# Kernel optimization log

Hardware: AMD Instinct MI355X
Metric: run time of the kernel (lower is better)

## Reference

```python
import jax, jax.numpy as jnp
import numpy as np

TOP_K = 2  # n_heads / k in SigmaMoE


def setup_inputs() -> dict:
    key = jax.random.key(0)
    k1, k2, k3, k4 = jax.random.split(key, 4)
    B, S, d = 4, 2048, 512
    E, H = 32, 128  # n_experts, expert_size
    # init scales mirror reset_parameters (std ~ 1/sqrt(fan_in)) so sigmoid router is unsaturated
    x = jax.random.normal(k1, (B, S, d), dtype=jnp.float32)
    expert_sel = jax.random.normal(k2, (E, d), dtype=jnp.float32) / np.sqrt(d).astype(np.float32)
    keys = jax.random.normal(k3, (E, d, H), dtype=jnp.float32) / np.sqrt(d).astype(np.float32)
    values = jax.random.normal(k4, (E, H, d), dtype=jnp.float32) / np.sqrt(E * H).astype(np.float32)
    return {"x": x, "expert_sel": expert_sel, "keys": keys, "values": values}


def reference(x, expert_sel, keys, values):
    # x: [B, S, d]; expert_sel: [E, d]; keys: [E, d, H]; values: [E, H, v]
    B, S, d = x.shape
    E = keys.shape[0]
    xt = x.reshape(-1, d)                       # [T, d] tokens
    T = xt.shape[0]

    # Router: sigmoid gate + top-k expert selection (eval mode: no dropout, no sel_hist)
    sel = jax.nn.sigmoid(xt @ expert_sel.T)     # [T, E]
    sel_val, sel_idx = jax.lax.top_k(sel, TOP_K)  # [T, K] each; combine is order-invariant

    # Sparse routing weights as dense [T, E] mask (zero for unselected experts,
    # so unselected expert compute is exactly cancelled -> same math as cvmm dispatch/combine)
    w = jnp.zeros((T, E), dtype=xt.dtype).at[jnp.arange(T)[:, None], sel_idx].add(sel_val)

    # Expert FFN: scores = relu(x @ keys[e]); out = sum_e w[t,e] * scores @ values[e]
    h = jax.nn.relu(jnp.einsum('td,edh->teh', xt, keys))   # [T, E, H]
    out = jnp.einsum('teh,te,ehv->tv', h, w, values)       # [T, v]
    return out.reshape(B, S, -1)
```

## Files before the change

### kernel.cpp

```cpp
#include <hip/hip_runtime.h>

#define TT 8192
#define DD 512
#define EE 32
#define HH 128

typedef float f32x4 __attribute__((ext_vector_type(4)));
typedef __bf16 bf16x8 __attribute__((ext_vector_type(8)));
typedef unsigned short u16x8 __attribute__((ext_vector_type(8)));

__device__ __forceinline__ unsigned short f2bf(float f) {
  unsigned int u = __builtin_bit_cast(unsigned int, f);
  u = (u + 0x7FFFu + ((u >> 16) & 1u)) >> 16;
  return (unsigned short)u;
}
__device__ __forceinline__ float bf2f(unsigned short h) {
  return __builtin_bit_cast(float, (unsigned int)h << 16);
}

#define GLD16(g, l)                                                            \
  __builtin_amdgcn_global_load_lds(                                            \
      (const __attribute__((address_space(1))) unsigned int*)(g),              \
      (__attribute__((address_space(3))) unsigned int*)(l), 16, 0, 0)

__global__ __launch_bounds__(256) void convert_kernel(
    const float* __restrict__ keys, const float* __restrict__ values,
    const float* __restrict__ esel,
    unsigned short* __restrict__ keysT, unsigned short* __restrict__ valuesT,
    unsigned short* __restrict__ eselF, int* __restrict__ cur) {
  __shared__ float tile[64][68];
  int bid = blockIdx.x;
  const int t = threadIdx.x;
  if (bid >= 1024) {
    if (bid == 1024 && t < EE) cur[t] = 0;
    int f = (bid - 1024) * 256 + t;
    int lane = f & 63;
    int rest = f >> 6;
    int half = rest & 1;
    int kt = rest >> 1;
    int term = kt % 3;
    int k = kt / 3;
    int n = half * 16 + (lane & 15);
    int col = k * 32 + (lane >> 4) * 8;
    const float* s = esel + (size_t)n * DD + col;
    unsigned short o[8];
#pragma unroll
    for (int q = 0; q < 8; q++) {
      float v = s[q];
      unsigned short hh = f2bf(v);
      float r1 = v - bf2f(hh);
      unsigned short lo = f2bf(r1);
      float r2 = r1 - bf2f(lo);
      o[q] = (term == 0) ? hh : (term == 1) ? lo : f2bf(r2);
    }
    *(u16x8*)(eselF + (size_t)f * 8) = *(const u16x8*)o;
    return;
  }
  const float* src;
  unsigned short* dst;
  int R, C, r0, c0, e;
  if (bid < 512) {
    e = bid >> 4; int sub = bid & 15;
    R = DD; C = HH; r0 = (sub >> 1) * 64; c0 = (sub & 1) * 64;
    src = keys; dst = keysT;
  } else {
    bid -= 512;
    e = bid >> 4; int sub = bid & 15;
    R = HH; C = DD; r0 = (sub & 1) * 64; c0 = (sub >> 1) * 64;
    src = values; dst = valuesT;
  }
  const int rl = t >> 2, cq = (t & 3) * 16;
  const float* s0 = src + ((size_t)e * R + r0 + rl) * C + c0 + cq;
#pragma unroll
  for (int i = 0; i < 4; i++) *(float4*)&tile[rl][cq + 4 * i] = *(const float4*)(s0 + 4 * i);
  __syncthreads();
  unsigned short* d0 = dst + ((size_t)e * C + c0 + rl) * R + r0 + cq;
#pragma unroll
  for (int i = 0; i < 4; i++) {
    ushort4 v;
    v.x = f2bf(tile[cq + 4 * i + 0][rl]);
    v.y = f2bf(tile[cq + 4 * i + 1][rl]);
    v.z = f2bf(tile[cq + 4 * i + 2][rl]);
    v.w = f2bf(tile[cq + 4 * i + 3][rl]);
    *(ushort4*)(d0 + 4 * i) = v;
  }
}

__global__ __launch_bounds__(256) void router_kernel(
    const float* __restrict__ x, const unsigned short* __restrict__ eselF,
    unsigned short* __restrict__ xb, int* __restrict__ etok,
    float* __restrict__ ew, int* __restrict__ cur) {
  __shared__ float ls[2][32][33];
  __shared__ int bcnt[EE], bbase[EE], bcur[EE];
  const int tid = threadIdx.x;
  const int tok0 = blockIdx.x * 32;
  const int wv = tid >> 6, lane = tid & 63;
  const int mh = wv & 1;
  const int kh2 = wv >> 1;
  const int ll = lane & 15, lh = lane >> 4;
  const int row = tok0 + mh * 16 + ll;

  const float* xr = x + (size_t)row * DD + lh * 8;
  unsigned short* xbr = xb + (size_t)row * DD + lh * 8;

  f32x4 acc0, acc1;
  acc0[0] = 0.f; acc0[1] = 0.f; acc0[2] = 0.f; acc0[3] = 0.f;
  acc1 = acc0;

  for (int kl = 0; kl < 8; kl++) {
    int k = kh2 * 8 + kl;
    float4 v0 = *(const float4*)(xr + k * 32);
    float4 v1 = *(const float4*)(xr + k * 32 + 4);
    float vv[8] = {v0.x, v0.y, v0.z, v0.w, v1.x, v1.y, v1.z, v1.w};
    bf16x8 ah, al, al2;
    unsigned short hs[8];
#pragma unroll
    for (int j = 0; j < 8; j++) {
      unsigned short hh = f2bf(vv[j]);
      float r1 = vv[j] - bf2f(hh);
      unsigned short lo = f2bf(r1);
      float r2 = r1 - bf2f(lo);
      hs[j] = hh;
      ah[j] = __builtin_bit_cast(__bf16, hh);
      al[j] = __builtin_bit_cast(__bf16, lo);
      al2[j] = __builtin_bit_cast(__bf16, f2bf(r2));
    }
    *(ushort4*)(xbr + k * 32) = *(ushort4*)&hs[0];
    *(ushort4*)(xbr + k * 32 + 4) = *(ushort4*)&hs[4];

    const unsigned short* fk = eselF + (size_t)k * 6 * 512 + lane * 8;
    bf16x8 bh0 = *(const bf16x8*)(fk);
    bf16x8 bh1 = *(const bf16x8*)(fk + 512);
    bf16x8 bl0 = *(const bf16x8*)(fk + 1024);
    bf16x8 bl1 = *(const bf16x8*)(fk + 1536);
    bf16x8 bm0 = *(const bf16x8*)(fk + 2048);
    bf16x8 bm1 = *(const bf16x8*)(fk + 2560);

    acc0 = __builtin_amdgcn_mfma_f32_16x16x32_bf16(ah, bh0, acc0, 0, 0, 0);
    acc0 = __builtin_amdgcn_mfma_f32_16x16x32_bf16(ah, bl0, acc0, 0, 0, 0);
    acc0 = __builtin_amdgcn_mfma_f32_16x16x32_bf16(al, bh0, acc0, 0, 0, 0);
    acc0 = __builtin_amdgcn_mfma_f32_16x16x32_bf16(ah, bm0, acc0, 0, 0, 0);
    acc0 = __builtin_amdgcn_mfma_f32_16x16x32_bf16(al, bl0, acc0, 0, 0, 0);
    acc0 = __builtin_amdgcn_mfma_f32_16x16x32_bf16(al2, bh0, acc0, 0, 0, 0);

    acc1 = __builtin_amdgcn_mfma_f32_16x16x32_bf16(ah, bh1, acc1, 0, 0, 0);
    acc1 = __builtin_amdgcn_mfma_f32_16x16x32_bf16(ah, bl1, acc1, 0, 0, 0);
    acc1 = __builtin_amdgcn_mfma_f32_16x16x32_bf16(al, bh1, acc1, 0, 0, 0);
    acc1 = __builtin_amdgcn_mfma_f32_16x16x32_bf16(ah, bm1, acc1, 0, 0, 0);
    acc1 = __builtin_amdgcn_mfma_f32_16x16x32_bf16(al, bl1, acc1, 0, 0, 0);
    acc1 = __builtin_amdgcn_mfma_f32_16x16x32_bf16(al2, bh1, acc1, 0, 0, 0);
  }

#pragma unroll
  for (int r = 0; r < 4; r++) {
    ls[kh2][mh * 16 + lh * 4 + r][ll] = acc0[r];
    ls[kh2][mh * 16 + lh * 4 + r][16 + ll] = acc1[r];
  }
  if (tid < EE) bcnt[tid] = 0;
  __syncthreads();

  int i0 = 0, i1 = 0;
  float w0 = 0.f, w1 = 0.f;
  if (tid < 32) {
    float m0 = -3.4e38f;
#pragma unroll
    for (int e2 = 0; e2 < EE; e2++) {
      float v = ls[0][tid][e2] + ls[1][tid][e2];
      if (v > m0) { m0 = v; i0 = e2; }
    }
    float m1 = -3.4e38f;
    i1 = (i0 == 0) ? 1 : 0;
#pragma unroll
    for (int e2 = 0; e2 < EE; e2++) {
      float v = ls[0][tid][e2] + ls[1][tid][e2];
      if (e2 != i0 && v > m1) { m1 = v; i1 = e2; }
    }
    w0 = 1.f / (1.f + expf(-m0));
    w1 = 1.f / (1.f + expf(-m1));
    atomicAdd(&bcnt[i0], 1);
    atomicAdd(&bcnt[i1], 1);
  }
  __syncthreads();
  if (tid < EE) { bbase[tid] = atomicAdd(&cur[tid], bcnt[tid]); bcur[tid] = 0; }
  __syncthreads();
  if (tid < 32) {
    int t = tok0 + tid;
    int p0 = bbase[i0] + atomicAdd(&bcur[i0], 1);
    etok[(size_t)i0 * TT + p0] = t;
    ew[(size_t)i0 * TT + p0] = w0;
    int p1 = bbase[i1] + atomicAdd(&bcur[i1], 1);
    etok[(size_t)i1 * TT + p1] = t | (1 << 20);
    ew[(size_t)i1 * TT + p1] = w1;
  }
}

__global__ __launch_bounds__(512) void moe_gemm_kernel(
    const unsigned short* __restrict__ xb,
    const unsigned short* __restrict__ keysT,
    const unsigned short* __restrict__ valuesT,
    const int* __restrict__ cur,
    const int* __restrict__ etok,
    const float* __restrict__ ew,
    unsigned short* __restrict__ yb) {
  const int e = blockIdx.x;
  const int cnt = cur[e];
  const int base = blockIdx.y * 64;
  if (base >= cnt) return;

  __shared__ unsigned short stage_buf[2][8192];
  __shared__ unsigned short h_swz[8192];
  __shared__ int tok_s[64];
  __shared__ int srow_s[64];
  __shared__ float w_s[64];

  const int tid = threadIdx.x;
  const int lane = tid & 63;
  const int wv = tid >> 6;
  const int wm = wv & 3;
  const int wn = wv >> 2;
  const int ll = lane & 15, lh = lane >> 4;

  const unsigned short* kT = keysT + (size_t)e * HH * DD;
  const unsigned short* vT = valuesT + (size_t)e * DD * HH;

  auto stage_b1 = [&](int c, int b) {
#pragma unroll
    for (int i = 0; i < 2; i++) {
      int P = (i * 512 + tid) * 16;
      int n = P >> 7;
      int q = P & 127;
      const char* g = (const char*)(kT + (size_t)n * DD + c * 64) + (q ^ ((n & 7) << 4));
      char* l = (char*)stage_buf[b] + (i * 512 + (tid & ~63)) * 16;
      GLD16(g, l);
    }
  };
  auto stage_b2 = [&](int c, int b) {
#pragma unroll
    for (int i = 0; i < 2; i++) {
      int P = (i * 512 + tid) * 16;
      int r = P >> 8;
      int q = P & 255;
      const char* g = (const char*)(vT + (size_t)(c * 64 + r) * HH) + (q ^ ((r & 7) << 4));
      char* l = (char*)stage_buf[b] + (i * 512 + (tid & ~63)) * 16;
      GLD16(g, l);
    }
  };

  stage_b1(0, 0);
  if (tid < 64) {
    int i = base + tid;
    if (i < cnt) {
      int v = etok[(size_t)e * TT + i];
      int t = v & 0xFFFFF;
      tok_s[tid] = t;
      srow_s[tid] = (v >> 20) * (TT + 1) + t;
      w_s[tid] = ew[(size_t)e * TT + i];
    } else {
      tok_s[tid] = etok[(size_t)e * TT + base] & 0xFFFFF;
      srow_s[tid] = TT;
      w_s[tid] = 0.f;
    }
  }
  __syncthreads();

  const unsigned short* ap = xb + (size_t)tok_s[wm * 16 + ll] * DD;

  f32x4 acc[4];
#pragma unroll
  for (int n = 0; n < 4; n++) { acc[n][0] = 0.f; acc[n][1] = 0.f; acc[n][2] = 0.f; acc[n][3] = 0.f; }

  for (int c = 0; c < 8; c++) {
    if (c < 7) stage_b1(c + 1, (c + 1) & 1);
    else       stage_b2(0, 0);
    const char* sb = (const char*)stage_buf[c & 1];
#pragma unroll
    for (int kkl = 0; kkl < 2; kkl++) {
      bf16x8 af = *(const bf16x8*)(ap + c * 64 + kkl * 32 + lh * 8);
#pragma unroll
      for (int nt = 0; nt < 4; nt++) {
        int n = wn * 64 + nt * 16 + ll;
        int boff = n * 128 + ((kkl * 64 + lh * 16) ^ ((n & 7) << 4));
        bf16x8 bfr = *(const bf16x8*)(sb + boff);
        acc[nt] = __builtin_amdgcn_mfma_f32_16x16x32_bf16(af, bfr, acc[nt], 0, 0, 0);
      }
    }
    __syncthreads();
  }

#pragma unroll
  for (int nt = 0; nt < 4; nt++) {
#pragma unroll
    for (int r = 0; r < 4; r++) {
      int row = wm * 16 + lh * 4 + r;
      int col = wn * 64 + nt * 16 + ll;
      int off = row * 256 + ((col * 2) ^ ((row & 7) << 4));
      *(unsigned short*)((char*)h_swz + off) = f2bf(fmaxf(acc[nt][r], 0.f));
    }
  }
  __syncthreads();

  bf16x8 a2[4];
#pragma unroll
  for (int kk = 0; kk < 4; kk++) {
    int row = wm * 16 + ll;
    int off = row * 256 + ((kk * 64 + lh * 16) ^ ((row & 7) << 4));
    a2[kk] = *(const bf16x8*)((const char*)h_swz + off);
  }

  float wr[4];
#pragma unroll
  for (int r = 0; r < 4; r++) wr[r] = w_s[wm * 16 + lh * 4 + r];

  __syncthreads();
  unsigned short* y_lds = h_swz;

  for (int c = 0; c < 8; c++) {
    if (c < 7) stage_b2(c + 1, (c + 1) & 1);
    const char* sb = (const char*)stage_buf[c & 1];
#pragma unroll
    for (int ntl = 0; ntl < 2; ntl++) {
      f32x4 c2;
      c2[0] = 0.f; c2[1] = 0.f; c2[2] = 0.f; c2[3] = 0.f;
#pragma unroll
      for (int kk = 0; kk < 4; kk++) {
        int r = wn * 32 + ntl * 16 + ll;
        int boff = r * 256 + ((kk * 64 + lh * 16) ^ ((r & 7) << 4));
        bf16x8 bfr = *(const bf16x8*)(sb + boff);
        c2 = __builtin_amdgcn_mfma_f32_16x16x32_bf16(a2[kk], bfr, c2, 0, 0, 0);
      }
      int colb = wn * 32 + ntl * 16 + ll;
#pragma unroll
      for (int r = 0; r < 4; r++) {
        int row = wm * 16 + lh * 4 + r;
        int off = row * 128 + ((colb * 2) ^ ((row & 7) << 4));
        *(unsigned short*)((char*)y_lds + off) = f2bf(c2[r] * wr[r]);
      }
    }
    __syncthreads();
    {
      int rr = tid >> 3, g = tid & 7;
      int off = rr * 128 + ((g * 16) ^ ((rr & 7) << 4));
      u16x8 v = *(const u16x8*)((const char*)y_lds + off);
      *(u16x8*)(yb + (size_t)srow_s[rr] * DD + c * 64 + g * 8) = v;
    }
    __syncthreads();
  }
}

__global__ __launch_bounds__(256) void combine_kernel(const unsigned short* __restrict__ yb,
                                                      float* __restrict__ out) {
  size_t i = ((size_t)blockIdx.x * 256 + threadIdx.x) * 8;
  u16x8 a = *(const u16x8*)(yb + i);
  u16x8 b = *(const u16x8*)(yb + (size_t)(TT + 1) * DD + i);
  float4 o0, o1;
  o0.x = bf2f(a[0]) + bf2f(b[0]);
  o0.y = bf2f(a[1]) + bf2f(b[1]);
  o0.z = bf2f(a[2]) + bf2f(b[2]);
  o0.w = bf2f(a[3]) + bf2f(b[3]);
  o1.x = bf2f(a[4]) + bf2f(b[4]);
  o1.y = bf2f(a[5]) + bf2f(b[5]);
  o1.z = bf2f(a[6]) + bf2f(b[6]);
  o1.w = bf2f(a[7]) + bf2f(b[7]);
  *(float4*)(out + i) = o0;
  *(float4*)(out + i + 4) = o1;
}

extern "C" void kernel_launch(void* const* d_in, const int* in_sizes, int n_in,
                              void* d_out, int out_size, void* d_ws, size_t ws_size,
                              hipStream_t stream) {
  const float* x = (const float*)d_in[0];
  const float* esel = (const float*)d_in[1];
  const float* keys = (const float*)d_in[2];
  const float* values = (const float*)d_in[3];
  float* out = (float*)d_out;

  char* p = (char*)d_ws;
  unsigned short* xb = (unsigned short*)p;      p += (size_t)TT * DD * 2;
  unsigned short* keysT = (unsigned short*)p;   p += (size_t)EE * DD * HH * 2;
  unsigned short* valuesT = (unsigned short*)p; p += (size_t)EE * DD * HH * 2;
  unsigned short* eselF = (unsigned short*)p;   p += (size_t)6144 * 8 * 2;
  int* cur = (int*)p;                           p += 256;
  int* etok = (int*)p;                          p += (size_t)EE * TT * 4;
  float* ew = (float*)p;                        p += (size_t)EE * TT * 4;
  unsigned short* yb = (unsigned short*)p;      p += (size_t)2 * (TT + 1) * DD * 2;

  convert_kernel<<<1048, 256, 0, stream>>>(keys, values, esel, keysT, valuesT, eselF, cur);
  router_kernel<<<TT / 32, 256, 0, stream>>>(x, eselF, xb, etok, ew, cur);
  moe_gemm_kernel<<<dim3(EE, TT / 64), 512, 0, stream>>>(xb, keysT, valuesT, cur, etok, ew, yb);
  combine_kernel<<<(TT * DD / 8) / 256, 256, 0, stream>>>(yb, out);
}
```

Before: 52.52 us.

## Fuse router into prep kernel and replace global atomics with per-block counts

Merges the router and the weight-conversion kernel into one launch. The router now splits expert_sel into three bf16 parts on the fly instead of reading a precomputed eselF buffer. The global atomic counters are replaced by per-block, per-expert counts written to a table. Each GEMM block rebuilds offsets with a 256-entry prefix scan and locates its tokens by binary search. This removes one kernel launch, the counter-reset dependency and the contended atomics, at the cost of redundant scan work in every GEMM block and repeated esel conversion in every router block.

Result: faster. 51.22 us (-2.5%).

```diff
diff --git a/kernel.cpp b/kernel.cpp
--- a/kernel.cpp
+++ b/kernel.cpp
@@ -4,6 +4,7 @@
 #define DD 512
 #define EE 32
 #define HH 128
+#define NRB 256
 
 typedef float f32x4 __attribute__((ext_vector_type(4)));
 typedef __bf16 bf16x8 __attribute__((ext_vector_type(8)));
@@ -23,39 +24,140 @@
       (const __attribute__((address_space(1))) unsigned int*)(g),              \
       (__attribute__((address_space(3))) unsigned int*)(l), 16, 0, 0)
 
-__global__ __launch_bounds__(256) void convert_kernel(
+__global__ __launch_bounds__(256) void prep_kernel(
+    const float* __restrict__ x, const float* __restrict__ esel,
     const float* __restrict__ keys, const float* __restrict__ values,
-    const float* __restrict__ esel,
     unsigned short* __restrict__ keysT, unsigned short* __restrict__ valuesT,
-    unsigned short* __restrict__ eselF, int* __restrict__ cur) {
+    unsigned short* __restrict__ xb, int* __restrict__ ccnt,
+    int* __restrict__ etok, float* __restrict__ ew) {
+  const int tid = threadIdx.x;
+  int bid = blockIdx.x;
+  if (bid < NRB) {
+    __shared__ float ls[2][32][33];
+    __shared__ int bcnt[EE], bcur[EE];
+    const int tok0 = bid * 32;
+    const int wv = tid >> 6, lane = tid & 63;
+    const int mh = wv & 1;
+    const int kh2 = wv >> 1;
+    const int ll = lane & 15, lh = lane >> 4;
+    const int row = tok0 + mh * 16 + ll;
+
+    const float* xr = x + (size_t)row * DD + lh * 8;
+    unsigned short* xbr = xb + (size_t)row * DD + lh * 8;
+    const float* e0 = esel + (size_t)ll * DD + lh * 8;
+    const float* e1 = esel + (size_t)(ll + 16) * DD + lh * 8;
+
+    f32x4 acc0, acc1;
+    acc0[0] = 0.f; acc0[1] = 0.f; acc0[2] = 0.f; acc0[3] = 0.f;
+    acc1 = acc0;
+
+#pragma unroll 2
+    for (int kl = 0; kl < 8; kl++) {
+      int k = kh2 * 8 + kl;
+      float4 v0 = *(const float4*)(xr + k * 32);
+      float4 v1 = *(const float4*)(xr + k * 32 + 4);
+      float vv[8] = {v0.x, v0.y, v0.z, v0.w, v1.x, v1.y, v1.z, v1.w};
+      bf16x8 ah, al, al2;
+      unsigned short hs[8];
+#pragma unroll
+      for (int j = 0; j < 8; j++) {
+        unsigned short hh = f2bf(vv[j]);
+        float r1 = vv[j] - bf2f(hh);
+        unsigned short lo = f2bf(r1);
+        float r2 = r1 - bf2f(lo);
+        hs[j] = hh;
+        ah[j] = __builtin_bit_cast(__bf16, hh);
+        al[j] = __builtin_bit_cast(__bf16, lo);
+        al2[j] = __builtin_bit_cast(__bf16, f2bf(r2));
+      }
+      *(ushort4*)(xbr + k * 32) = *(ushort4*)&hs[0];
+      *(ushort4*)(xbr + k * 32 + 4) = *(ushort4*)&hs[4];
+
+      float4 c00 = *(const float4*)(e0 + k * 32);
+      float4 c01 = *(const float4*)(e0 + k * 32 + 4);
+      float4 c10 = *(const float4*)(e1 + k * 32);
+      float4 c11 = *(const float4*)(e1 + k * 32 + 4);
+      float ea[8] = {c00.x, c00.y, c00.z, c00.w, c01.x, c01.y, c01.z, c01.w};
+      float eb[8] = {c10.x, c10.y, c10.z, c10.w, c11.x, c11.y, c11.z, c11.w};
+      bf16x8 bh0, bl0, bm0, bh1, bl1, bm1;
+#pragma unroll
+      for (int j = 0; j < 8; j++) {
+        unsigned short hh = f2bf(ea[j]);
+        float r1 = ea[j] - bf2f(hh);
+        unsigned short lo = f2bf(r1);
+        float r2 = r1 - bf2f(lo);
+        bh0[j] = __builtin_bit_cast(__bf16, hh);
+        bl0[j] = __builtin_bit_cast(__bf16, lo);
+        bm0[j] = __builtin_bit_cast(__bf16, f2bf(r2));
+        hh = f2bf(eb[j]);
+        r1 = eb[j] - bf2f(hh);
+        lo = f2bf(r1);
+        r2 = r1 - bf2f(lo);
+        bh1[j] = __builtin_bit_cast(__bf16, hh);
+        bl1[j] = __builtin_bit_cast(__bf16, lo);
+        bm1[j] = __builtin_bit_cast(__bf16, f2bf(r2));
+      }
+
+      acc0 = __builtin_amdgcn_mfma_f32_16x16x32_bf16(ah, bh0, acc0, 0, 0, 0);
+      acc0 = __builtin_amdgcn_mfma_f32_16x16x32_bf16(ah, bl0, acc0, 0, 0, 0);
+      acc0 = __builtin_amdgcn_mfma_f32_16x16x32_bf16(al, bh0, acc0, 0, 0, 0);
+      acc0 = __builtin_amdgcn_mfma_f32_16x16x32_bf16(ah, bm0, acc0, 0, 0, 0);
+      acc0 = __builtin_amdgcn_mfma_f32_16x16x32_bf16(al, bl0, acc0, 0, 0, 0);
+      acc0 = __builtin_amdgcn_mfma_f32_16x16x32_bf16(al2, bh0, acc0, 0, 0, 0);
+
+      acc1 = __builtin_amdgcn_mfma_f32_16x16x32_bf16(ah, bh1, acc1, 0, 0, 0);
+      acc1 = __builtin_amdgcn_mfma_f32_16x16x32_bf16(ah, bl1, acc1, 0, 0, 0);
+      acc1 = __builtin_amdgcn_mfma_f32_16x16x32_bf16(al, bh1, acc1, 0, 0, 0);
+      acc1 = __builtin_amdgcn_mfma_f32_16x16x32_bf16(ah, bm1, acc1, 0, 0, 0);
+      acc1 = __builtin_amdgcn_mfma_f32_16x16x32_bf16(al, bl1, acc1, 0, 0, 0);
+      acc1 = __builtin_amdgcn_mfma_f32_16x16x32_bf16(al2, bh1, acc1, 0, 0, 0);
+    }
+
+#pragma unroll
+    for (int r = 0; r < 4; r++) {
+      ls[kh2][mh * 16 + lh * 4 + r][ll] = acc0[r];
+      ls[kh2][mh * 16 + lh * 4 + r][16 + ll] = acc1[r];
+    }
+    if (tid < EE) bcnt[tid] = 0;
+    __syncthreads();
+
+    int i0 = 0, i1 = 0;
+    float w0 = 0.f, w1 = 0.f;
+    if (tid < 32) {
+      float m0 = -3.4e38f;
+#pragma unroll
+      for (int e2 = 0; e2 < EE; e2++) {
+        float v = ls[0][tid][e2] + ls[1][tid][e2];
+        if (v > m0) { m0 = v; i0 = e2; }
+      }
+      float m1 = -3.4e38f;
+      i1 = (i0 == 0) ? 1 : 0;
+#pragma unroll
+      for (int e2 = 0; e2 < EE; e2++) {
+        float v = ls[0][tid][e2] + ls[1][tid][e2];
+        if (e2 != i0 && v > m1) { m1 = v; i1 = e2; }
+      }
+      w0 = 1.f / (1.f + expf(-m0));
+      w1 = 1.f / (1.f + expf(-m1));
+      atomicAdd(&bcnt[i0], 1);
+      atomicAdd(&bcnt[i1], 1);
+    }
+    __syncthreads();
+    if (tid < EE) { ccnt[tid * NRB + bid] = bcnt[tid]; bcur[tid] = 0; }
+    __syncthreads();
+    if (tid < 32) {
+      int t = tok0 + tid;
+      int p0 = atomicAdd(&bcur[i0], 1);
+      etok[((size_t)i0 * NRB + bid) * 32 + p0] = t;
+      ew[((size_t)i0 * NRB + bid) * 32 + p0] = w0;
+      int p1 = atomicAdd(&bcur[i1], 1);
+      etok[((size_t)i1 * NRB + bid) * 32 + p1] = t | (1 << 20);
+      ew[((size_t)i1 * NRB + bid) * 32 + p1] = w1;
+    }
+    return;
+  }
+  bid -= NRB;
   __shared__ float tile[64][68];
-  int bid = blockIdx.x;
-  const int t = threadIdx.x;
-  if (bid >= 1024) {
-    if (bid == 1024 && t < EE) cur[t] = 0;
-    int f = (bid - 1024) * 256 + t;
-    int lane = f & 63;
-    int rest = f >> 6;
-    int half = rest & 1;
-    int kt = rest >> 1;
-    int term = kt % 3;
-    int k = kt / 3;
-    int n = half * 16 + (lane & 15);
-    int col = k * 32 + (lane >> 4) * 8;
-    const float* s = esel + (size_t)n * DD + col;
-    unsigned short o[8];
-#pragma unroll
-    for (int q = 0; q < 8; q++) {
-      float v = s[q];
-      unsigned short hh = f2bf(v);
-      float r1 = v - bf2f(hh);
-      unsigned short lo = f2bf(r1);
-      float r2 = r1 - bf2f(lo);
-      o[q] = (term == 0) ? hh : (term == 1) ? lo : f2bf(r2);
-    }
-    *(u16x8*)(eselF + (size_t)f * 8) = *(const u16x8*)o;
-    return;
-  }
   const float* src;
   unsigned short* dst;
   int R, C, r0, c0, e;
@@ -69,7 +171,7 @@
     R = HH; C = DD; r0 = (sub & 1) * 64; c0 = (sub >> 1) * 64;
     src = values; dst = valuesT;
   }
-  const int rl = t >> 2, cq = (t & 3) * 16;
+  const int rl = tid >> 2, cq = (tid & 3) * 16;
   const float* s0 = src + ((size_t)e * R + r0 + rl) * C + c0 + cq;
 #pragma unroll
   for (int i = 0; i < 4; i++) *(float4*)&tile[rl][cq + 4 * i] = *(const float4*)(s0 + 4 * i);
@@ -86,127 +188,18 @@
   }
 }
 
-__global__ __launch_bounds__(256) void router_kernel(
-    const float* __restrict__ x, const unsigned short* __restrict__ eselF,
-    unsigned short* __restrict__ xb, int* __restrict__ etok,
-    float* __restrict__ ew, int* __restrict__ cur) {
-  __shared__ float ls[2][32][33];
-  __shared__ int bcnt[EE], bbase[EE], bcur[EE];
-  const int tid = threadIdx.x;
-  const int tok0 = blockIdx.x * 32;
-  const int wv = tid >> 6, lane = tid & 63;
-  const int mh = wv & 1;
-  const int kh2 = wv >> 1;
-  const int ll = lane & 15, lh = lane >> 4;
-  const int row = tok0 + mh * 16 + ll;
-
-  const float* xr = x + (size_t)row * DD + lh * 8;
-  unsigned short* xbr = xb + (size_t)row * DD + lh * 8;
-
-  f32x4 acc0, acc1;
-  acc0[0] = 0.f; acc0[1] = 0.f; acc0[2] = 0.f; acc0[3] = 0.f;
-  acc1 = acc0;
-
-  for (int kl = 0; kl < 8; kl++) {
-    int k = kh2 * 8 + kl;
-    float4 v0 = *(const float4*)(xr + k * 32);
-    float4 v1 = *(const float4*)(xr + k * 32 + 4);
-    float vv[8] = {v0.x, v0.y, v0.z, v0.w, v1.x, v1.y, v1.z, v1.w};
-    bf16x8 ah, al, al2;
-    unsigned short hs[8];
-#pragma unroll
-    for (int j = 0; j < 8; j++) {
-      unsigned short hh = f2bf(vv[j]);
-      float r1 = vv[j] - bf2f(hh);
-      unsigned short lo = f2bf(r1);
-      float r2 = r1 - bf2f(lo);
-      hs[j] = hh;
-      ah[j] = __builtin_bit_cast(__bf16, hh);
-      al[j] = __builtin_bit_cast(__bf16, lo);
-      al2[j] = __builtin_bit_cast(__bf16, f2bf(r2));
-    }
-    *(ushort4*)(xbr + k * 32) = *(ushort4*)&hs[0];
-    *(ushort4*)(xbr + k * 32 + 4) = *(ushort4*)&hs[4];
-
-    const unsigned short* fk = eselF + (size_t)k * 6 * 512 + lane * 8;
-    bf16x8 bh0 = *(const bf16x8*)(fk);
-    bf16x8 bh1 = *(const bf16x8*)(fk + 512);
-    bf16x8 bl0 = *(const bf16x8*)(fk + 1024);
-    bf16x8 bl1 = *(const bf16x8*)(fk + 1536);
-    bf16x8 bm0 = *(const bf16x8*)(fk + 2048);
-    bf16x8 bm1 = *(const bf16x8*)(fk + 2560);
-
-    acc0 = __builtin_amdgcn_mfma_f32_16x16x32_bf16(ah, bh0, acc0, 0, 0, 0);
-    acc0 = __builtin_amdgcn_mfma_f32_16x16x32_bf16(ah, bl0, acc0, 0, 0, 0);
-    acc0 = __builtin_amdgcn_mfma_f32_16x16x32_bf16(al, bh0, acc0, 0, 0, 0);
-    acc0 = __builtin_amdgcn_mfma_f32_16x16x32_bf16(ah, bm0, acc0, 0, 0, 0);
-    acc0 = __builtin_amdgcn_mfma_f32_16x16x32_bf16(al, bl0, acc0, 0, 0, 0);
-    acc0 = __builtin_amdgcn_mfma_f32_16x16x32_bf16(al2, bh0, acc0, 0, 0, 0);
-
-    acc1 = __builtin_amdgcn_mfma_f32_16x16x32_bf16(ah, bh1, acc1, 0, 0, 0);
-    acc1 = __builtin_amdgcn_mfma_f32_16x16x32_bf16(ah, bl1, acc1, 0, 0, 0);
-    acc1 = __builtin_amdgcn_mfma_f32_16x16x32_bf16(al, bh1, acc1, 0, 0, 0);
-    acc1 = __builtin_amdgcn_mfma_f32_16x16x32_bf16(ah, bm1, acc1, 0, 0, 0);
-    acc1 = __builtin_amdgcn_mfma_f32_16x16x32_bf16(al, bl1, acc1, 0, 0, 0);
-    acc1 = __builtin_amdgcn_mfma_f32_16x16x32_bf16(al2, bh1, acc1, 0, 0, 0);
-  }
-
-#pragma unroll
-  for (int r = 0; r < 4; r++) {
-    ls[kh2][mh * 16 + lh * 4 + r][ll] = acc0[r];
-    ls[kh2][mh * 16 + lh * 4 + r][16 + ll] = acc1[r];
-  }
-  if (tid < EE) bcnt[tid] = 0;
-  __syncthreads();
-
-  int i0 = 0, i1 = 0;
-  float w0 = 0.f, w1 = 0.f;
-  if (tid < 32) {
-    float m0 = -3.4e38f;
-#pragma unroll
-    for (int e2 = 0; e2 < EE; e2++) {
-      float v = ls[0][tid][e2] + ls[1][tid][e2];
-      if (v > m0) { m0 = v; i0 = e2; }
-    }
-    float m1 = -3.4e38f;
-    i1 = (i0 == 0) ? 1 : 0;
-#pragma unroll
-    for (int e2 = 0; e2 < EE; e2++) {
-      float v = ls[0][tid][e2] + ls[1][tid][e2];
-      if (e2 != i0 && v > m1) { m1 = v; i1 = e2; }
-    }
-    w0 = 1.f / (1.f + expf(-m0));
-    w1 = 1.f / (1.f + expf(-m1));
-    atomicAdd(&bcnt[i0], 1);
-    atomicAdd(&bcnt[i1], 1);
-  }
-  __syncthreads();
-  if (tid < EE) { bbase[tid] = atomicAdd(&cur[tid], bcnt[tid]); bcur[tid] = 0; }
-  __syncthreads();
-  if (tid < 32) {
-    int t = tok0 + tid;
-    int p0 = bbase[i0] + atomicAdd(&bcur[i0], 1);
-    etok[(size_t)i0 * TT + p0] = t;
-    ew[(size_t)i0 * TT + p0] = w0;
-    int p1 = bbase[i1] + atomicAdd(&bcur[i1], 1);
-    etok[(size_t)i1 * TT + p1] = t | (1 << 20);
-    ew[(size_t)i1 * TT + p1] = w1;
-  }
-}
-
 __global__ __launch_bounds__(512) void moe_gemm_kernel(
     const unsigned short* __restrict__ xb,
     const unsigned short* __restrict__ keysT,
     const unsigned short* __restrict__ valuesT,
-    const int* __restrict__ cur,
+    const int* __restrict__ ccnt,
     const int* __restrict__ etok,
     const float* __restrict__ ew,
     unsigned short* __restrict__ yb) {
   const int e = blockIdx.x;
-  const int cnt = cur[e];
   const int base = blockIdx.y * 64;
-  if (base >= cnt) return;
-
+
+  __shared__ int csc[NRB];
   __shared__ unsigned short stage_buf[2][8192];
   __shared__ unsigned short h_swz[8192];
   __shared__ int tok_s[64];
@@ -214,6 +207,19 @@
   __shared__ float w_s[64];
 
   const int tid = threadIdx.x;
+
+  if (tid < NRB) csc[tid] = ccnt[e * NRB + tid];
+  __syncthreads();
+  for (int off = 1; off < NRB; off <<= 1) {
+    int v = 0;
+    if (tid < NRB) { v = csc[tid]; if (tid >= off) v += csc[tid - off]; }
+    __syncthreads();
+    if (tid < NRB) csc[tid] = v;
+    __syncthreads();
+  }
+  const int cnt = csc[NRB - 1];
+  if (base >= cnt) return;
+
   const int lane = tid & 63;
   const int wv = tid >> 6;
   const int wm = wv & 3;
@@ -249,17 +255,17 @@
   stage_b1(0, 0);
   if (tid < 64) {
     int i = base + tid;
-    if (i < cnt) {
-      int v = etok[(size_t)e * TT + i];
-      int t = v & 0xFFFFF;
-      tok_s[tid] = t;
-      srow_s[tid] = (v >> 20) * (TT + 1) + t;
-      w_s[tid] = ew[(size_t)e * TT + i];
-    } else {
-      tok_s[tid] = etok[(size_t)e * TT + base] & 0xFFFFF;
-      srow_s[tid] = TT;
-      w_s[tid] = 0.f;
-    }
+    bool valid = i < cnt;
+    int ie = valid ? i : (cnt - 1);
+    int lo = 0, hi = NRB - 1;
+    while (lo < hi) { int mid = (lo + hi) >> 1; if (csc[mid] > ie) hi = mid; else lo = mid + 1; }
+    int prev = lo ? csc[lo - 1] : 0;
+    size_t cell = ((size_t)e * NRB + lo) * 32 + (ie - prev);
+    int v = etok[cell];
+    int t = v & 0xFFFFF;
+    tok_s[tid] = t;
+    srow_s[tid] = valid ? ((v >> 20) * (TT + 1) + t) : TT;
+    w_s[tid] = valid ? ew[cell] : 0.f;
   }
   __syncthreads();
 
@@ -378,14 +384,13 @@
   unsigned short* xb = (unsigned short*)p;      p += (size_t)TT * DD * 2;
   unsigned short* keysT = (unsigned short*)p;   p += (size_t)EE * DD * HH * 2;
   unsigned short* valuesT = (unsigned short*)p; p += (size_t)EE * DD * HH * 2;
-  unsigned short* eselF = (unsigned short*)p;   p += (size_t)6144 * 8 * 2;
-  int* cur = (int*)p;                           p += 256;
-  int* etok = (int*)p;                          p += (size_t)EE * TT * 4;
-  float* ew = (float*)p;                        p += (size_t)EE * TT * 4;
+  int* ccnt = (int*)p;                          p += (size_t)EE * NRB * 4;
+  int* etok = (int*)p;                          p += (size_t)EE * NRB * 32 * 4;
+  float* ew = (float*)p;                        p += (size_t)EE * NRB * 32 * 4;
   unsigned short* yb = (unsigned short*)p;      p += (size_t)2 * (TT + 1) * DD * 2;
 
-  convert_kernel<<<1048, 256, 0, stream>>>(keys, values, esel, keysT, valuesT, eselF, cur);
-  router_kernel<<<TT / 32, 256, 0, stream>>>(x, eselF, xb, etok, ew, cur);
-  moe_gemm_kernel<<<dim3(EE, TT / 64), 512, 0, stream>>>(xb, keysT, valuesT, cur, etok, ew, yb);
+  prep_kernel<<<NRB + 1024, 256, 0, stream>>>(x, esel, keys, values, keysT, valuesT,
+                                              xb, ccnt, etok, ew);
+  moe_gemm_kernel<<<dim3(EE, TT / 64), 512, 0, stream>>>(xb, keysT, valuesT, ccnt, etok, ew, yb);
   combine_kernel<<<(TT * DD / 8) / 256, 256, 0, stream>>>(yb, out);
 }
```
